# Performance work log

Measured on AMD Instinct MI355X. Metric: run time of the kernel, lower is better.

Reference implementation:

```python
import jax, jax.numpy as jnp
import numpy as np

K_BASE = 8
K_MAX = 20
NUM_GROUPS = 16  # min(32, 64 // 4)
EPS = 1e-5


def _knn_idx_adaptive(x, mask, k_base=K_BASE, k_max=K_MAX):
    # x: [B, N, D] float, mask: [B, N] bool. Returns idx: [B, N, k_max] int32.
    B, N, D = x.shape
    x2 = jnp.sum(x * x, axis=-1, keepdims=True)              # [B, N, 1]
    dist2 = x2 + x2.transpose(0, 2, 1) - 2.0 * jnp.einsum('bnd,bmd->bnm', x, x)
    dist2 = jnp.clip(dist2, 0.0)
    valid = mask[:, :, None] & mask[:, None, :]
    eye = jnp.eye(N, dtype=bool)[None]
    dist2 = jnp.where(valid & ~eye, dist2, jnp.inf)
    counts = mask.sum(axis=1)                                 # [B]
    k_per = jnp.clip(jnp.sqrt(counts.astype(jnp.float32) / 50.0) * k_base,
                     k_base, k_max).astype(jnp.int32)         # truncation == torch .long()
    k_global = jnp.minimum(k_max, jnp.maximum(1, counts.min() - 1))
    _, idx = jax.lax.top_k(-dist2, k_max)                     # [B, N, k_max]
    first_valid = jnp.argmax(mask, axis=1)                    # [B]
    cols = jnp.arange(k_max)[None, None, :]
    k_eff = jnp.minimum(k_per, k_global)[:, None, None]
    # cols < k_eff: true top-k neighbors; [k_eff, k_global): repeat first valid; >= k_global: pad 0
    idx = jnp.where(cols < k_eff, idx,
                    jnp.where(cols < k_global, first_valid[:, None, None], 0))
    return idx


def _group_norm(h, gamma, beta, num_groups=NUM_GROUPS, eps=EPS):
    # h: [..., C]
    shp = h.shape
    C = shp[-1]
    hg = h.reshape(shp[:-1] + (num_groups, C // num_groups))
    mu = hg.mean(axis=-1, keepdims=True)
    var = hg.var(axis=-1, keepdims=True)
    hg = (hg - mu) * jax.lax.rsqrt(var + eps)
    return hg.reshape(shp) * gamma + beta


def setup_inputs() -> dict:
    key = jax.random.key(0)
    kx, kl, k1, k2 = jax.random.split(key, 4)
    B, N, D, C = 16, 1024, 64, 64
    x = jax.random.normal(kx, (B, N, D), dtype=jnp.float32)
    lengths = jax.random.randint(kl, (B,), 256, N + 1)
    mask = jnp.arange(N)[None, :] < lengths[:, None]          # [B, N] bool
    W1 = jax.random.normal(k1, (2 * D, C), dtype=jnp.float32) / np.sqrt(2 * D)
    b1 = jnp.zeros((C,), dtype=jnp.float32)
    gamma = jnp.ones((C,), dtype=jnp.float32)
    beta = jnp.zeros((C,), dtype=jnp.float32)
    W2 = jax.random.normal(k2, (C, C), dtype=jnp.float32) / np.sqrt(C)
    b2 = jnp.zeros((C,), dtype=jnp.float32)
    return {"x": x, "mask": mask, "W1": W1, "b1": b1,
            "gamma": gamma, "beta": beta, "W2": W2, "b2": b2}


def reference(x, mask, W1, b1, gamma, beta, W2, b2):
    B, N, D = x.shape
    idx = _knn_idx_adaptive(x, mask)                          # [B, N, k]
    k = idx.shape[-1]
    x_nb = jnp.take_along_axis(x[:, :, None, :].repeat(1, axis=2),
                               idx[..., None], axis=1) if False else \
        x[jnp.arange(B)[:, None, None], idx]                  # [B, N, k, D]
    x_i = jnp.broadcast_to(x[:, :, None, :], (B, N, k, D))
    edge = jnp.concatenate([x_i, x_nb - x_i], axis=-1)        # [B, N, k, 2D]
    h = jax.nn.relu(_group_norm(edge @ W1 + b1, gamma, beta)) # [B, N, k, C]
    h = h @ W2 + b2
    out = h.max(axis=2)                                       # [B, N, C]
    return out * mask[..., None].astype(out.dtype)
```

## Files before the change

### kernel.cpp

```cpp
#include <hip/hip_runtime.h>
#include <stdint.h>

#define BB 16
#define NN 1024
#define DD 64
#define CC 64
#define KMAX 20
#define ROWS 8

typedef unsigned long long u64;
typedef float f32x2 __attribute__((ext_vector_type(2)));
typedef float f32x4v __attribute__((ext_vector_type(4)));
typedef short bf16x8 __attribute__((ext_vector_type(8)));

__device__ inline u64 umin64(u64 a, u64 b) { return a < b ? a : b; }

__device__ inline unsigned f2bf(float f) {
    unsigned u = __float_as_uint(f);
    return (u + 0x7FFFu + ((u >> 16) & 1u)) >> 16;
}

__device__ inline bf16x8 pack8(const float4 a, const float4 b) {
    union { unsigned u[4]; bf16x8 v; } r;
    r.u[0] = f2bf(a.x) | (f2bf(a.y) << 16);
    r.u[1] = f2bf(a.z) | (f2bf(a.w) << 16);
    r.u[2] = f2bf(b.x) | (f2bf(b.y) << 16);
    r.u[3] = f2bf(b.z) | (f2bf(b.w) << 16);
    return r.v;
}

struct bfpair { bf16x8 hi, lo; };
__device__ __forceinline__ bfpair split8(const float v[8]) {
    union { unsigned u[4]; bf16x8 x; } H, L;
#pragma unroll
    for (int i = 0; i < 4; ++i) {
        unsigned h0 = f2bf(v[2 * i]), h1 = f2bf(v[2 * i + 1]);
        float r0 = v[2 * i] - __uint_as_float(h0 << 16);
        float r1 = v[2 * i + 1] - __uint_as_float(h1 << 16);
        H.u[i] = h0 | (h1 << 16);
        L.u[i] = f2bf(r0) | (f2bf(r1) << 16);
    }
    bfpair r; r.hi = H.x; r.lo = L.x; return r;
}

__device__ inline void gn4(float4& h, const float4 g, const float4 be) {
    float mu = (h.x + h.y + h.z + h.w) * 0.25f;
    float dx = h.x - mu, dy = h.y - mu, dz = h.z - mu, dw = h.w - mu;
    float var = (dx * dx + dy * dy + dz * dz + dw * dw) * 0.25f;
    float rs = __builtin_amdgcn_rsqf(var + 1e-5f);
    h.x = fmaxf(fmaf(dx * rs, g.x, be.x), 0.f);
    h.y = fmaxf(fmaf(dy * rs, g.y, be.y), 0.f);
    h.z = fmaxf(fmaf(dz * rs, g.z, be.z), 0.f);
    h.w = fmaxf(fmaf(dw * rs, g.w, be.w), 0.f);
}

__global__ __launch_bounds__(256) void k1_all(const float* __restrict__ x,
                                              const float* __restrict__ W1,
                                              const float* __restrict__ b1,
                                              float* __restrict__ base,
                                              float* __restrict__ fb,
                                              float* __restrict__ xT,
                                              float* __restrict__ x2,
                                              const void* __restrict__ maskp,
                                              int* __restrict__ counts,
                                              int* __restrict__ keff) {
    __shared__ float sXT[16][65];
    __shared__ int scnt[BB];
    int w = threadIdx.x >> 6, lane = threadIdx.x & 63;
    int lg = lane >> 4, lr = lane & 15;
    int p0 = blockIdx.x * 16;

    float av[8];
    bfpair A[2];
    {
        const float* xr = x + (size_t)(p0 + lr) * DD;
#pragma unroll
        for (int kt = 0; kt < 2; ++kt) {
            float4 a0 = *(const float4*)(xr + kt * 32 + lg * 8);
            float4 a1 = *(const float4*)(xr + kt * 32 + lg * 8 + 4);
            av[0] = a0.x; av[1] = a0.y; av[2] = a0.z; av[3] = a0.w;
            av[4] = a1.x; av[5] = a1.y; av[6] = a1.z; av[7] = a1.w;
            A[kt] = split8(av);
        }
    }
    bfpair Wa[2], Wb[2];
#pragma unroll
    for (int kt = 0; kt < 2; ++kt) {
        const float* wpa = W1 + (size_t)(kt * 32 + lg * 8) * CC + w * 16 + lr;
        float wv[8];
#pragma unroll
        for (int e = 0; e < 8; ++e) wv[e] = wpa[e * CC];
        Wa[kt] = split8(wv);
        const float* wpb = wpa + (size_t)DD * CC;
#pragma unroll
        for (int e = 0; e < 8; ++e) wv[e] = wpb[e * CC];
        Wb[kt] = split8(wv);
    }
    f32x4v P = {0, 0, 0, 0}, Q = {0, 0, 0, 0};
#pragma unroll
    for (int kt = 0; kt < 2; ++kt) {
        P = __builtin_amdgcn_mfma_f32_16x16x32_bf16(A[kt].hi, Wa[kt].hi, P, 0, 0, 0);
        P = __builtin_amdgcn_mfma_f32_16x16x32_bf16(A[kt].hi, Wa[kt].lo, P, 0, 0, 0);
        P = __builtin_amdgcn_mfma_f32_16x16x32_bf16(A[kt].lo, Wa[kt].hi, P, 0, 0, 0);
        Q = __builtin_amdgcn_mfma_f32_16x16x32_bf16(A[kt].hi, Wb[kt].hi, Q, 0, 0, 0);
        Q = __builtin_amdgcn_mfma_f32_16x16x32_bf16(A[kt].hi, Wb[kt].lo, Q, 0, 0, 0);
        Q = __builtin_amdgcn_mfma_f32_16x16x32_bf16(A[kt].lo, Wb[kt].hi, Q, 0, 0, 0);
    }
    {
        float b1c = b1[w * 16 + lr];
#pragma unroll
        for (int r = 0; r < 4; ++r) {
            size_t off = (size_t)(p0 + lg * 4 + r) * CC + w * 16 + lr;
            base[off] = P[r] - Q[r] + b1c;
            fb[off] = Q[r];
        }
    }

#pragma unroll
    for (int q = 0; q < 4; ++q) {
        int pl = w * 4 + q;
        float xv = x[((size_t)(p0 + pl) << 6) + lane];
        sXT[pl][lane] = xv;
        float sq = xv * xv;
        for (int off = 32; off; off >>= 1) sq += __shfl_xor(sq, off);
        if (lane == 0) x2[p0 + pl] = sq;
    }
    __syncthreads();
    {
        int t = threadIdx.x;
        int b = p0 >> 10, nb = p0 & 1023;
        int d = t >> 2, q4 = (t & 3) << 2;
        float4 v;
        v.x = sXT[q4 + 0][d]; v.y = sXT[q4 + 1][d]; v.z = sXT[q4 + 2][d]; v.w = sXT[q4 + 3][d];
        *(float4*)&xT[(((size_t)(b << 6) + d) << 10) + nb + q4] = v;
    }

    if (blockIdx.x == 0) {
        const unsigned char* mb = (const unsigned char*)maskp;
        const int* mi = (const int*)maskp;
        bool bytelayout = (mb[1] != 0);
        for (int bq = 0; bq < 4; ++bq) {
            int bb = w * 4 + bq;
            int s = 0;
            for (int i = 0; i < 16; ++i) {
                int nn2 = lane + (i << 6);
                int v = bytelayout ? (mb[bb * NN + nn2] ? 1 : 0)
                                   : (mi[bb * NN + nn2] ? 1 : 0);
                s += v;
            }
            for (int off = 32; off; off >>= 1) s += __shfl_xor(s, off);
            if (lane == 0) scnt[bb] = s;
        }
        __syncthreads();
        int t = threadIdx.x;
        if (t < BB) {
            int minc = scnt[0];
            for (int qq = 1; qq < BB; ++qq) minc = min(minc, scnt[qq]);
            int kglob = min(KMAX, max(1, minc - 1));
            float c = (float)scnt[t];
            float v = sqrtf(c / 50.0f) * 8.0f;
            v = fminf(fmaxf(v, 8.0f), 20.0f);
            int kper = (int)v;
            counts[t] = scnt[t];
            keff[t] = min(kper, kglob);
        }
    }
}

#define CE(a, b)                                                      \
    {                                                                 \
        bool sw_ = pk[b] < pk[a];                                     \
        u64 ta_ = pk[a];                                              \
        pk[a] = sw_ ? pk[b] : pk[a];                                  \
        pk[b] = sw_ ? ta_ : pk[b];                                    \
    }

__device__ __forceinline__ u64 head16(const u64 (&pk)[16]) {
    u64 h01 = umin64(pk[0], pk[1]),   h23 = umin64(pk[2], pk[3]);
    u64 h45 = umin64(pk[4], pk[5]),   h67 = umin64(pk[6], pk[7]);
    u64 h89 = umin64(pk[8], pk[9]),   hab = umin64(pk[10], pk[11]);
    u64 hcd = umin64(pk[12], pk[13]), hef = umin64(pk[14], pk[15]);
    return umin64(umin64(umin64(h01, h23), umin64(h45, h67)),
                  umin64(umin64(h89, hab), umin64(hcd, hef)));
}

__device__ __forceinline__ int sortpop(u64 (&pk)[16], int kef, int lane) {
    CE(0,1) CE(2,3) CE(4,5) CE(6,7) CE(8,9) CE(10,11) CE(12,13) CE(14,15)
    CE(0,2) CE(1,3) CE(4,6) CE(5,7) CE(8,10) CE(9,11) CE(12,14) CE(13,15)
    CE(1,2) CE(5,6) CE(9,10) CE(13,14)
    CE(0,4) CE(1,5) CE(2,6) CE(3,7) CE(8,12) CE(9,13) CE(10,14) CE(11,15)
    CE(2,4) CE(3,5) CE(10,12) CE(11,13)
    CE(1,2) CE(3,4) CE(5,6) CE(9,10) CE(11,12) CE(13,14)
    CE(0,8) CE(1,9) CE(2,10) CE(3,11) CE(4,12) CE(5,13) CE(6,14) CE(7,15)
    CE(4,8) CE(5,9) CE(6,10) CE(7,11)
    CE(2,4) CE(3,5) CE(6,8) CE(7,9) CE(10,12) CE(11,13)
    CE(1,2) CE(3,4) CE(5,6) CE(7,8) CE(9,10) CE(11,12) CE(13,14)
    u64 myhead = pk[0];
    int my_m = 0;
    for (int j = 0; j < kef; ++j) {
        u64 g = myhead;
        for (int off = 32; off; off >>= 1) {
            u64 o = __shfl_xor(g, off);
            g = (o < g) ? o : g;
        }
        my_m = (j == lane) ? (int)(unsigned)(g & 0xffffffffu) : my_m;
        bool win = (myhead == g);
#pragma unroll
        for (int tt = 0; tt < 15; ++tt) pk[tt] = win ? pk[tt + 1] : pk[tt];
        pk[15] = win ? ~0ULL : pk[15];
        myhead = pk[0];
    }
    return my_m;
}

#define ROWFMA(r, rv, cv)                                                        \
    {                                                                            \
        axy[r] = __builtin_elementwise_fma((f32x2){rv, rv}, (f32x2){cv.x, cv.y}, \
                                           axy[r]);                              \
        azw[r] = __builtin_elementwise_fma((f32x2){rv, rv}, (f32x2){cv.z, cv.w}, \
                                           azw[r]);                              \
    }

__global__ __launch_bounds__(256) void k2_knn(const float* __restrict__ x,
                                              const float* __restrict__ xT,
                                              const float* __restrict__ x2,
                                              const int* __restrict__ counts,
                                              const int* __restrict__ keff,
                                              int* __restrict__ idx) {
    __shared__ float sD[ROWS][NN];
    int b = blockIdx.x >> 7;
    int n0 = (blockIdx.x & 127) * ROWS;
    int cnt = counts[b];
    if (n0 >= cnt) return;
    int kef = keff[b];
    int w = threadIdx.x >> 6, lane = threadIdx.x & 63;
    const float* x2b = x2 + (b << 10);

    if ((w << 8) < cnt) {
        f32x2 axy[ROWS], azw[ROWS];
#pragma unroll
        for (int r = 0; r < ROWS; ++r) { axy[r] = (f32x2){0.f, 0.f}; azw[r] = (f32x2){0.f, 0.f}; }
        const float* xTb = xT + ((size_t)b << 16);
        const float* xrow0 = x + ((size_t)(b << 10) + n0) * DD;
        int c0 = (w << 8) + (lane << 2);
        for (int d0 = 0; d0 < DD; d0 += 4) {
            float4 cv0 = *(const float4*)(xTb + ((size_t)(d0 + 0) << 10) + c0);
            float4 cv1 = *(const float4*)(xTb + ((size_t)(d0 + 1) << 10) + c0);
            float4 cv2 = *(const float4*)(xTb + ((size_t)(d0 + 2) << 10) + c0);
            float4 cv3 = *(const float4*)(xTb + ((size_t)(d0 + 3) << 10) + c0);
#pragma unroll
            for (int r = 0; r < ROWS; ++r) {
                float4 rv = *(const float4*)(xrow0 + r * DD + d0);
                ROWFMA(r, rv.x, cv0)
                ROWFMA(r, rv.y, cv1)
                ROWFMA(r, rv.z, cv2)
                ROWFMA(r, rv.w, cv3)
            }
        }
#pragma unroll
        for (int r = 0; r < ROWS; ++r)
            *(float4*)&sD[r][c0] = make_float4(axy[r].x, axy[r].y, azw[r].x, azw[r].y);
    }
    __syncthreads();

    int rA = w, rB = w + 4;
    int nA = n0 + rA, nB = n0 + rB;
    bool vA = nA < cnt, vB = nB < cnt;
    if (!vA) return;
    float x2A = x2b[nA];
    float x2B = x2b[nB & 1023];
    u64 pkA[16], pkB[16];
#pragma unroll
    for (int tt = 0; tt < 16; ++tt) {
        int c = (tt << 6) + lane;
        float xc = x2b[c];
        float dA = fmaxf((x2A + xc) - 2.0f * sD[rA][c], 0.0f);
        float dB = fmaxf((x2B + xc) - 2.0f * sD[rB][c], 0.0f);
        pkA[tt] = (c < cnt && c != nA)
            ? (((u64)__float_as_uint(dA) << 32) | (unsigned)c) : ~0ULL;
        pkB[tt] = (vB && c < cnt && c != nB)
            ? (((u64)__float_as_uint(dB) << 32) | (unsigned)c) : ~0ULL;
    }
    u64 hA = head16(pkA), hB = head16(pkB);
    unsigned hTA = (unsigned)(hA >> 48), hTB = (unsigned)(hB >> 48);
    unsigned prefA = 0u, prefB = 0u;
    int rankA = kef, rankB = kef;
#pragma unroll
    for (int bbit = 15; bbit >= 0; --bbit) {
        unsigned bitm = 1u << bbit;
        bool cA = (((hTA ^ prefA) >> (bbit + 1)) == 0) && ((hTA & bitm) == 0);
        bool cB = (((hTB ^ prefB) >> (bbit + 1)) == 0) && ((hTB & bitm) == 0);
        u64 mA = __ballot(cA);
        u64 mB = __ballot(cB);
        int nA0 = __popcll(mA), nB0 = __popcll(mB);
        if (rankA > nA0) { rankA -= nA0; prefA |= bitm; }
        if (rankB > nB0) { rankB -= nB0; prefB |= bitm; }
    }
    u64 t0A = ((u64)((prefA << 16) | 0xFFFFu) << 32) | 0xFFFFFFFFULL;
    u64 t0B = vB ? (((u64)((prefB << 16) | 0xFFFFu) << 32) | 0xFFFFFFFFULL) : 0ULL;

    u64* svA = (u64*)&sD[rA][0];
    u64* svB = (u64*)&sD[rB][0];
    u64 lmask = (lane == 0) ? 0ULL : ((~0ULL) >> (64 - lane));
    int SA = 0, SB = 0;
#pragma unroll
    for (int i = 0; i < 16; ++i) {
        bool qA = (pkA[i] <= t0A);
        bool qB = (pkB[i] <= t0B);
        u64 mA = __ballot(qA);
        u64 mB = __ballot(qB);
        if (qA) svA[SA + __popcll(mA & lmask)] = pkA[i];
        if (qB) svB[SB + __popcll(mB & lmask)] = pkB[i];
        SA += __popcll(mA);
        SB += __popcll(mB);
    }
    size_t prowA = (size_t)(b << 10) + nA;
    size_t prowB = (size_t)(b << 10) + nB;
    if (SA <= 64 && SB <= 64) {
        u64 sA = (lane < SA) ? svA[lane] : ~0ULL;
        u64 sB = (lane < SB) ? svB[lane] : ~0ULL;
        int rkA = 0, rkB = 0;
        int SM = max(SA, SB);
        for (int j = 0; j < SM; ++j) {
            u64 aj = svA[j];
            u64 bj = svB[j];
            rkA += (j < SA && aj < sA) ? 1 : 0;
            rkB += (j < SB && bj < sB) ? 1 : 0;
        }
        if (rkA < kef && lane < SA) idx[prowA * KMAX + rkA] = (int)(unsigned)(sA & 0xffffffffu);
        if (lane >= kef && lane < KMAX) idx[prowA * KMAX + lane] = 0;
        if (vB) {
            if (rkB < kef && lane < SB) idx[prowB * KMAX + rkB] = (int)(unsigned)(sB & 0xffffffffu);
            if (lane >= kef && lane < KMAX) idx[prowB * KMAX + lane] = 0;
        }
    } else {
        int mA = sortpop(pkA, kef, lane);
        if (lane < KMAX) idx[prowA * KMAX + lane] = (lane < kef) ? mA : 0;
        if (vB) {
            int mB = sortpop(pkB, kef, lane);
            if (lane < KMAX) idx[prowB * KMAX + lane] = (lane < kef) ? mB : 0;
        }
    }
}

__global__ __launch_bounds__(256, 2) void k3_mlp(const float* __restrict__ base,
                                                 const float* __restrict__ fb,
                                                 const int* __restrict__ idx,
                                                 const int* __restrict__ counts,
                                                 const float* __restrict__ gamma,
                                                 const float* __restrict__ beta,
                                                 const float* __restrict__ W2,
                                                 const float* __restrict__ b2,
                                                 float* __restrict__ out) {
    __shared__ float sC[4][64][20];
    int w = threadIdx.x >> 6, lane = threadIdx.x & 63;
    int lg = lane >> 4, lr = lane & 15;
    int p0 = blockIdx.x * 16;
    int b = p0 >> 10;
    int n0b = p0 & 1023;
    int cnt = counts[b];
    int pt = p0 + lr;
    bool aval = (n0b + lr) < cnt;

    bf16x8 Bf[4][2];
#pragma unroll
    for (int nt = 0; nt < 4; ++nt)
#pragma unroll
        for (int kt = 0; kt < 2; ++kt) {
            float4 lo, hi;
            const float* wp = W2 + (size_t)(kt * 32 + lg * 8) * CC + nt * 16 + lr;
            lo.x = wp[0 * CC]; lo.y = wp[1 * CC]; lo.z = wp[2 * CC]; lo.w = wp[3 * CC];
            hi.x = wp[4 * CC]; hi.y = wp[5 * CC]; hi.z = wp[6 * CC]; hi.w = wp[7 * CC];
            Bf[nt][kt] = pack8(lo, hi);
        }

    const float* bp = base + (size_t)pt * CC + lg * 8;
    float4 baA0 = *(const float4*)(bp);
    float4 baA1 = *(const float4*)(bp + 4);
    float4 baB0 = *(const float4*)(bp + 32);
    float4 baB1 = *(const float4*)(bp + 36);
    const float* gp = gamma + lg * 8;
    float4 gA0 = *(const float4*)(gp),      gA1 = *(const float4*)(gp + 4);
    float4 gB0 = *(const float4*)(gp + 32), gB1 = *(const float4*)(gp + 36);
    const float* bep = beta + lg * 8;
    float4 eA0 = *(const float4*)(bep),      eA1 = *(const float4*)(bep + 4);
    float4 eB0 = *(const float4*)(bep + 32), eB1 = *(const float4*)(bep + 36);

    const float* fbb = fb + ((size_t)(b << 10)) * CC;
    const int* idxp = idx + (size_t)pt * KMAX;

    f32x4v cmax[4];
#pragma unroll
    for (int nt = 0; nt < 4; ++nt) cmax[nt] = (f32x4v){-1e30f, -1e30f, -1e30f, -1e30f};

#pragma unroll
    for (int jj = 0; jj < 5; ++jj) {
        int j = w * 5 + jj;
        int m = aval ? idxp[j] : 0;
        const float* fr = fbb + (size_t)m * CC + lg * 8;
        float4 hA0 = *(const float4*)(fr);
        float4 hA1 = *(const float4*)(fr + 4);
        float4 hB0 = *(const float4*)(fr + 32);
        float4 hB1 = *(const float4*)(fr + 36);
        hA0.x += baA0.x; hA0.y += baA0.y; hA0.z += baA0.z; hA0.w += baA0.w;
        hA1.x += baA1.x; hA1.y += baA1.y; hA1.z += baA1.z; hA1.w += baA1.w;
        hB0.x += baB0.x; hB0.y += baB0.y; hB0.z += baB0.z; hB0.w += baB0.w;
        hB1.x += baB1.x; hB1.y += baB1.y; hB1.z += baB1.z; hB1.w += baB1.w;
        gn4(hA0, gA0, eA0);
        gn4(hA1, gA1, eA1);
        gn4(hB0, gB0, eB0);
        gn4(hB1, gB1, eB1);
        bf16x8 A0 = pack8(hA0, hA1);
        bf16x8 A1 = pack8(hB0, hB1);
#pragma unroll
        for (int nt = 0; nt < 4; ++nt) {
            f32x4v c = {0.f, 0.f, 0.f, 0.f};
            c = __builtin_amdgcn_mfma_f32_16x16x32_bf16(A0, Bf[nt][0], c, 0, 0, 0);
            c = __builtin_amdgcn_mfma_f32_16x16x32_bf16(A1, Bf[nt][1], c, 0, 0, 0);
            cmax[nt].x = fmaxf(cmax[nt].x, c.x);
            cmax[nt].y = fmaxf(cmax[nt].y, c.y);
            cmax[nt].z = fmaxf(cmax[nt].z, c.z);
            cmax[nt].w = fmaxf(cmax[nt].w, c.w);
        }
    }
#pragma unroll
    for (int nt = 0; nt < 4; ++nt)
        *(float4*)&sC[w][lane][nt * 4] = (float4){cmax[nt].x, cmax[nt].y, cmax[nt].z, cmax[nt].w};
    __syncthreads();
    float b2c = b2[lane];
#pragma unroll
    for (int q = 0; q < 4; ++q) {
        int R = w * 4 + q;
        int src = ((R >> 2) << 4) + lr;
        int reg = (lg << 2) + (R & 3);
        float v = fmaxf(fmaxf(sC[0][src][reg], sC[1][src][reg]),
                        fmaxf(sC[2][src][reg], sC[3][src][reg]));
        bool valid = (n0b + R) < cnt;
        out[(size_t)(p0 + R) * CC + lane] = valid ? (v + b2c) : 0.f;
    }
}

extern "C" void kernel_launch(void* const* d_in, const int* in_sizes, int n_in,
                              void* d_out, int out_size, void* d_ws, size_t ws_size,
                              hipStream_t stream) {
    const float* x     = (const float*)d_in[0];
    const void*  maskp = d_in[1];
    const float* W1    = (const float*)d_in[2];
    const float* b1    = (const float*)d_in[3];
    const float* gamma = (const float*)d_in[4];
    const float* beta  = (const float*)d_in[5];
    const float* W2    = (const float*)d_in[6];
    const float* b2    = (const float*)d_in[7];
    float* out = (float*)d_out;

    int* d_counts = (int*)d_ws;
    int* d_keff   = d_counts + 16;
    float* d_x2   = (float*)(d_counts + 32);
    float* d_base = d_x2 + BB * NN;
    float* d_fb   = d_base + (size_t)BB * NN * CC;
    int* d_idx    = (int*)(d_fb + (size_t)BB * NN * CC);
    float* d_xT   = (float*)d_out;

    hipLaunchKernelGGL(k1_all, dim3(BB * NN / 16), dim3(256), 0, stream,
                       x, W1, b1, d_base, d_fb, d_xT, d_x2, maskp, d_counts, d_keff);
    hipLaunchKernelGGL(k2_knn, dim3(BB * (NN / ROWS)), dim3(256), 0, stream,
                       x, d_xT, d_x2, d_counts, d_keff, d_idx);
    hipLaunchKernelGGL(k3_mlp, dim3(BB * NN / 16), dim3(256), 0, stream,
                       d_base, d_fb, d_idx, d_counts, gamma, beta, W2, b2, out);
}
```

Measured before the change: 88.38 us.

## Compute kNN distances with bf16-split MFMA and 16-bit keys, refine exactly

The kNN distance matrix is now computed with split-bf16 MFMA (hi/lo, three products) over 16-row tiles instead of scalar FMA on a transposed copy of x, so the transpose in the first kernel is dropped. Distances are stored in shared memory as truncated 16-bit keys. A radix threshold search on those keys picks candidates, and the candidates are re-ranked with exact fp32 dot products. This removes the xT traffic and puts the dot products on matrix cores, but adds a per-row refinement pass and a full exact fallback whenever more than 64 candidates survive.

New measurement: 118.6 us. +34.2%, slower.

```diff
diff --git a/kernel.cpp b/kernel.cpp
--- a/kernel.cpp
+++ b/kernel.cpp
@@ -6,14 +6,11 @@
 #define DD 64
 #define CC 64
 #define KMAX 20
-#define ROWS 8
 
 typedef unsigned long long u64;
 typedef float f32x2 __attribute__((ext_vector_type(2)));
 typedef float f32x4v __attribute__((ext_vector_type(4)));
 typedef short bf16x8 __attribute__((ext_vector_type(8)));
-
-__device__ inline u64 umin64(u64 a, u64 b) { return a < b ? a : b; }
 
 __device__ inline unsigned f2bf(float f) {
     unsigned u = __float_as_uint(f);
@@ -54,17 +51,15 @@
     h.w = fmaxf(fmaf(dw * rs, g.w, be.w), 0.f);
 }
 
-__global__ __launch_bounds__(256) void k1_all(const float* __restrict__ x,
-                                              const float* __restrict__ W1,
-                                              const float* __restrict__ b1,
-                                              float* __restrict__ base,
-                                              float* __restrict__ fb,
-                                              float* __restrict__ xT,
-                                              float* __restrict__ x2,
-                                              const void* __restrict__ maskp,
-                                              int* __restrict__ counts,
-                                              int* __restrict__ keff) {
-    __shared__ float sXT[16][65];
+__global__ __launch_bounds__(256) void k1a_feats(const float* __restrict__ x,
+                                                 const float* __restrict__ W1,
+                                                 const float* __restrict__ b1,
+                                                 float* __restrict__ base,
+                                                 float* __restrict__ fb,
+                                                 float* __restrict__ x2,
+                                                 const void* __restrict__ maskp,
+                                                 int* __restrict__ counts,
+                                                 int* __restrict__ keff) {
     __shared__ int scnt[BB];
     int w = threadIdx.x >> 6, lane = threadIdx.x & 63;
     int lg = lane >> 4, lr = lane & 15;
@@ -96,6 +91,7 @@
         for (int e = 0; e < 8; ++e) wv[e] = wpb[e * CC];
         Wb[kt] = split8(wv);
     }
+
     f32x4v P = {0, 0, 0, 0}, Q = {0, 0, 0, 0};
 #pragma unroll
     for (int kt = 0; kt < 2; ++kt) {
@@ -118,21 +114,11 @@
 
 #pragma unroll
     for (int q = 0; q < 4; ++q) {
-        int pl = w * 4 + q;
+        int pl = (w << 2) + q;
         float xv = x[((size_t)(p0 + pl) << 6) + lane];
-        sXT[pl][lane] = xv;
         float sq = xv * xv;
         for (int off = 32; off; off >>= 1) sq += __shfl_xor(sq, off);
         if (lane == 0) x2[p0 + pl] = sq;
-    }
-    __syncthreads();
-    {
-        int t = threadIdx.x;
-        int b = p0 >> 10, nb = p0 & 1023;
-        int d = t >> 2, q4 = (t & 3) << 2;
-        float4 v;
-        v.x = sXT[q4 + 0][d]; v.y = sXT[q4 + 1][d]; v.z = sXT[q4 + 2][d]; v.w = sXT[q4 + 3][d];
-        *(float4*)&xT[(((size_t)(b << 6) + d) << 10) + nb + q4] = v;
     }
 
     if (blockIdx.x == 0) {
@@ -174,15 +160,6 @@
         pk[a] = sw_ ? pk[b] : pk[a];                                  \
         pk[b] = sw_ ? ta_ : pk[b];                                    \
     }
-
-__device__ __forceinline__ u64 head16(const u64 (&pk)[16]) {
-    u64 h01 = umin64(pk[0], pk[1]),   h23 = umin64(pk[2], pk[3]);
-    u64 h45 = umin64(pk[4], pk[5]),   h67 = umin64(pk[6], pk[7]);
-    u64 h89 = umin64(pk[8], pk[9]),   hab = umin64(pk[10], pk[11]);
-    u64 hcd = umin64(pk[12], pk[13]), hef = umin64(pk[14], pk[15]);
-    return umin64(umin64(umin64(h01, h23), umin64(h45, h67)),
-                  umin64(umin64(h89, hab), umin64(hcd, hef)));
-}
 
 __device__ __forceinline__ int sortpop(u64 (&pk)[16], int kef, int lane) {
     CE(0,1) CE(2,3) CE(4,5) CE(6,7) CE(8,9) CE(10,11) CE(12,13) CE(14,15)
@@ -213,132 +190,178 @@
     return my_m;
 }
 
-#define ROWFMA(r, rv, cv)                                                        \
-    {                                                                            \
-        axy[r] = __builtin_elementwise_fma((f32x2){rv, rv}, (f32x2){cv.x, cv.y}, \
-                                           axy[r]);                              \
-        azw[r] = __builtin_elementwise_fma((f32x2){rv, rv}, (f32x2){cv.z, cv.w}, \
-                                           azw[r]);                              \
-    }
+__device__ __forceinline__ float exact_dist(const float* __restrict__ xrow_lds,
+                                            const float* __restrict__ xc,
+                                            float x2n, float x2c) {
+    float dot = 0.f;
+#pragma unroll
+    for (int d4 = 0; d4 < 16; ++d4) {
+        float4 cv = *(const float4*)(xc + (d4 << 2));
+        float4 rv = *(const float4*)(xrow_lds + (d4 << 2));
+        dot = fmaf(rv.x, cv.x, dot);
+        dot = fmaf(rv.y, cv.y, dot);
+        dot = fmaf(rv.z, cv.z, dot);
+        dot = fmaf(rv.w, cv.w, dot);
+    }
+    return fmaxf((x2n + x2c) - 2.0f * dot, 0.0f);
+}
 
 __global__ __launch_bounds__(256) void k2_knn(const float* __restrict__ x,
-                                              const float* __restrict__ xT,
                                               const float* __restrict__ x2,
                                               const int* __restrict__ counts,
                                               const int* __restrict__ keff,
                                               int* __restrict__ idx) {
-    __shared__ float sD[ROWS][NN];
-    int b = blockIdx.x >> 7;
-    int n0 = (blockIdx.x & 127) * ROWS;
+    __shared__ unsigned short sDa[NN][16];
+    __shared__ float sXrow[16][64];
+    __shared__ unsigned sSv[16][64];
+    __shared__ u64 sEx[16][64];
+    int b = blockIdx.x >> 6;
+    int n0 = (blockIdx.x & 63) << 4;
     int cnt = counts[b];
     if (n0 >= cnt) return;
     int kef = keff[b];
     int w = threadIdx.x >> 6, lane = threadIdx.x & 63;
+    int lg = lane >> 4, lr = lane & 15;
+    const float* xb = x + (((size_t)(b << 10)) << 6);
     const float* x2b = x2 + (b << 10);
 
+    {
+        int t = threadIdx.x;
+        int row = t >> 4, d4 = (t & 15) << 2;
+        *(float4*)&sXrow[row][d4] = *(const float4*)(xb + (size_t)(n0 + row) * DD + d4);
+    }
+
+    bfpair A[2];
+    {
+        const float* xr = xb + (size_t)(n0 + lr) * DD;
+        float av[8];
+#pragma unroll
+        for (int kt = 0; kt < 2; ++kt) {
+            float4 a0 = *(const float4*)(xr + kt * 32 + lg * 8);
+            float4 a1 = *(const float4*)(xr + kt * 32 + lg * 8 + 4);
+            av[0] = a0.x; av[1] = a0.y; av[2] = a0.z; av[3] = a0.w;
+            av[4] = a1.x; av[5] = a1.y; av[6] = a1.z; av[7] = a1.w;
+            A[kt] = split8(av);
+        }
+    }
+    float x2r[4];
+#pragma unroll
+    for (int r = 0; r < 4; ++r) x2r[r] = x2b[n0 + lg * 4 + r];
+
     if ((w << 8) < cnt) {
-        f32x2 axy[ROWS], azw[ROWS];
-#pragma unroll
-        for (int r = 0; r < ROWS; ++r) { axy[r] = (f32x2){0.f, 0.f}; azw[r] = (f32x2){0.f, 0.f}; }
-        const float* xTb = xT + ((size_t)b << 16);
-        const float* xrow0 = x + ((size_t)(b << 10) + n0) * DD;
-        int c0 = (w << 8) + (lane << 2);
-        for (int d0 = 0; d0 < DD; d0 += 4) {
-            float4 cv0 = *(const float4*)(xTb + ((size_t)(d0 + 0) << 10) + c0);
-            float4 cv1 = *(const float4*)(xTb + ((size_t)(d0 + 1) << 10) + c0);
-            float4 cv2 = *(const float4*)(xTb + ((size_t)(d0 + 2) << 10) + c0);
-            float4 cv3 = *(const float4*)(xTb + ((size_t)(d0 + 3) << 10) + c0);
-#pragma unroll
-            for (int r = 0; r < ROWS; ++r) {
-                float4 rv = *(const float4*)(xrow0 + r * DD + d0);
-                ROWFMA(r, rv.x, cv0)
-                ROWFMA(r, rv.y, cv1)
-                ROWFMA(r, rv.z, cv2)
-                ROWFMA(r, rv.w, cv3)
+        for (int tile = 0; tile < 16; ++tile) {
+            int c = (w << 8) + (tile << 4) + lr;
+            const float* xc = xb + (size_t)c * DD;
+            bfpair Bf[2];
+            float bv[8];
+#pragma unroll
+            for (int kt = 0; kt < 2; ++kt) {
+                float4 b0 = *(const float4*)(xc + kt * 32 + lg * 8);
+                float4 b1v = *(const float4*)(xc + kt * 32 + lg * 8 + 4);
+                bv[0] = b0.x; bv[1] = b0.y; bv[2] = b0.z; bv[3] = b0.w;
+                bv[4] = b1v.x; bv[5] = b1v.y; bv[6] = b1v.z; bv[7] = b1v.w;
+                Bf[kt] = split8(bv);
             }
-        }
-#pragma unroll
-        for (int r = 0; r < ROWS; ++r)
-            *(float4*)&sD[r][c0] = make_float4(axy[r].x, axy[r].y, azw[r].x, azw[r].y);
+            f32x4v D = {0, 0, 0, 0};
+#pragma unroll
+            for (int kt = 0; kt < 2; ++kt) {
+                D = __builtin_amdgcn_mfma_f32_16x16x32_bf16(A[kt].hi, Bf[kt].hi, D, 0, 0, 0);
+                D = __builtin_amdgcn_mfma_f32_16x16x32_bf16(A[kt].hi, Bf[kt].lo, D, 0, 0, 0);
+                D = __builtin_amdgcn_mfma_f32_16x16x32_bf16(A[kt].lo, Bf[kt].hi, D, 0, 0, 0);
+            }
+            float x2c = x2b[c];
+            u64 pk4 = 0;
+#pragma unroll
+            for (int r = 0; r < 4; ++r) {
+                float da = fmaxf((x2r[r] + x2c) - 2.0f * D[r], 0.0f);
+                pk4 |= (u64)(__float_as_uint(da) >> 16) << (16 * r);
+            }
+            *(u64*)&sDa[c][lg << 2] = pk4;
+        }
     }
     __syncthreads();
 
-    int rA = w, rB = w + 4;
-    int nA = n0 + rA, nB = n0 + rB;
-    bool vA = nA < cnt, vB = nB < cnt;
-    if (!vA) return;
-    float x2A = x2b[nA];
-    float x2B = x2b[nB & 1023];
-    u64 pkA[16], pkB[16];
+    u64 vv[16];
 #pragma unroll
     for (int tt = 0; tt < 16; ++tt) {
         int c = (tt << 6) + lane;
-        float xc = x2b[c];
-        float dA = fmaxf((x2A + xc) - 2.0f * sD[rA][c], 0.0f);
-        float dB = fmaxf((x2B + xc) - 2.0f * sD[rB][c], 0.0f);
-        pkA[tt] = (c < cnt && c != nA)
-            ? (((u64)__float_as_uint(dA) << 32) | (unsigned)c) : ~0ULL;
-        pkB[tt] = (vB && c < cnt && c != nB)
-            ? (((u64)__float_as_uint(dB) << 32) | (unsigned)c) : ~0ULL;
-    }
-    u64 hA = head16(pkA), hB = head16(pkB);
-    unsigned hTA = (unsigned)(hA >> 48), hTB = (unsigned)(hB >> 48);
-    unsigned prefA = 0u, prefB = 0u;
-    int rankA = kef, rankB = kef;
+        vv[tt] = *(const u64*)&sDa[c][w << 2];
+    }
+    unsigned hmin[4] = {0xFFFFu, 0xFFFFu, 0xFFFFu, 0xFFFFu};
+#pragma unroll
+    for (int tt = 0; tt < 16; ++tt) {
+        int c = (tt << 6) + lane;
+        bool cv = c < cnt;
+#pragma unroll
+        for (int r = 0; r < 4; ++r) {
+            int n_r = n0 + (w << 2) + r;
+            unsigned key = (unsigned)((vv[tt] >> (16 * r)) & 0xFFFFu);
+            bool ok = cv && (c != n_r);
+            hmin[r] = (ok && key < hmin[r]) ? key : hmin[r];
+        }
+    }
+    unsigned pref[4] = {0, 0, 0, 0};
+    int rnk[4] = {kef, kef, kef, kef};
 #pragma unroll
     for (int bbit = 15; bbit >= 0; --bbit) {
         unsigned bitm = 1u << bbit;
-        bool cA = (((hTA ^ prefA) >> (bbit + 1)) == 0) && ((hTA & bitm) == 0);
-        bool cB = (((hTB ^ prefB) >> (bbit + 1)) == 0) && ((hTB & bitm) == 0);
-        u64 mA = __ballot(cA);
-        u64 mB = __ballot(cB);
-        int nA0 = __popcll(mA), nB0 = __popcll(mB);
-        if (rankA > nA0) { rankA -= nA0; prefA |= bitm; }
-        if (rankB > nB0) { rankB -= nB0; prefB |= bitm; }
-    }
-    u64 t0A = ((u64)((prefA << 16) | 0xFFFFu) << 32) | 0xFFFFFFFFULL;
-    u64 t0B = vB ? (((u64)((prefB << 16) | 0xFFFFu) << 32) | 0xFFFFFFFFULL) : 0ULL;
-
-    u64* svA = (u64*)&sD[rA][0];
-    u64* svB = (u64*)&sD[rB][0];
+#pragma unroll
+        for (int r = 0; r < 4; ++r) {
+            bool cnd = (((hmin[r] ^ pref[r]) >> (bbit + 1)) == 0) && !(hmin[r] & bitm);
+            u64 m = __ballot(cnd);
+            int c0n = __popcll(m);
+            if (rnk[r] > c0n) { rnk[r] -= c0n; pref[r] |= bitm; }
+        }
+    }
+    unsigned thr16[4];
+#pragma unroll
+    for (int r = 0; r < 4; ++r) {
+        float tup = __uint_as_float((pref[r] << 16) | 0xFFFFu) + 1.0f;
+        thr16[r] = __float_as_uint(tup) >> 16;
+    }
     u64 lmask = (lane == 0) ? 0ULL : ((~0ULL) >> (64 - lane));
-    int SA = 0, SB = 0;
-#pragma unroll
-    for (int i = 0; i < 16; ++i) {
-        bool qA = (pkA[i] <= t0A);
-        bool qB = (pkB[i] <= t0B);
-        u64 mA = __ballot(qA);
-        u64 mB = __ballot(qB);
-        if (qA) svA[SA + __popcll(mA & lmask)] = pkA[i];
-        if (qB) svB[SB + __popcll(mB & lmask)] = pkB[i];
-        SA += __popcll(mA);
-        SB += __popcll(mB);
-    }
-    size_t prowA = (size_t)(b << 10) + nA;
-    size_t prowB = (size_t)(b << 10) + nB;
-    if (SA <= 64 && SB <= 64) {
-        u64 sA = (lane < SA) ? svA[lane] : ~0ULL;
-        u64 sB = (lane < SB) ? svB[lane] : ~0ULL;
-        int rkA = 0, rkB = 0;
-        int SM = max(SA, SB);
-        for (int j = 0; j < SM; ++j) {
-            u64 aj = svA[j];
-            u64 bj = svB[j];
-            rkA += (j < SA && aj < sA) ? 1 : 0;
-            rkB += (j < SB && bj < sB) ? 1 : 0;
-        }
-        if (rkA < kef && lane < SA) idx[prowA * KMAX + rkA] = (int)(unsigned)(sA & 0xffffffffu);
-        if (lane >= kef && lane < KMAX) idx[prowA * KMAX + lane] = 0;
-        if (vB) {
-            if (rkB < kef && lane < SB) idx[prowB * KMAX + rkB] = (int)(unsigned)(sB & 0xffffffffu);
-            if (lane >= kef && lane < KMAX) idx[prowB * KMAX + lane] = 0;
-        }
-    } else {
-        int mA = sortpop(pkA, kef, lane);
-        if (lane < KMAX) idx[prowA * KMAX + lane] = (lane < kef) ? mA : 0;
-        if (vB) {
-            int mB = sortpop(pkB, kef, lane);
-            if (lane < KMAX) idx[prowB * KMAX + lane] = (lane < kef) ? mB : 0;
+    int S[4] = {0, 0, 0, 0};
+#pragma unroll
+    for (int tt = 0; tt < 16; ++tt) {
+        int c = (tt << 6) + lane;
+        bool cv = c < cnt;
+#pragma unroll
+        for (int r = 0; r < 4; ++r) {
+            int n_r = n0 + (w << 2) + r;
+            unsigned key = (unsigned)((vv[tt] >> (16 * r)) & 0xFFFFu);
+            bool q = cv && (c != n_r) && (n_r < cnt) && (key <= thr16[r]);
+            u64 m = __ballot(q);
+            if (q) sSv[(w << 2) + r][S[r] + __popcll(m & lmask)] = (unsigned)c;
+            S[r] += __popcll(m);
+        }
+    }
+    for (int r = 0; r < 4; ++r) {
+        int rloc = (w << 2) + r;
+        int n_r = n0 + rloc;
+        if (n_r >= cnt) continue;
+        size_t prow = (size_t)(b << 10) + n_r;
+        int Sr = S[r];
+        float x2n = x2b[n_r];
+        if (Sr <= 64) {
+            int c = (lane < Sr) ? (int)sSv[rloc][lane] : 0;
+            float de = exact_dist(&sXrow[rloc][0], xb + (size_t)c * DD, x2n, x2b[c]);
+            u64 key = (lane < Sr) ? (((u64)__float_as_uint(de) << 32) | (unsigned)c)
+                                  : ~0ULL;
+            sEx[rloc][lane] = key;
+            int rk = 0;
+            for (int j = 0; j < Sr; ++j) rk += (sEx[rloc][j] < key) ? 1 : 0;
+            if (rk < kef && lane < Sr) idx[prow * KMAX + rk] = c;
+            if (lane >= kef && lane < KMAX) idx[prow * KMAX + lane] = 0;
+        } else {
+            u64 pk[16];
+            for (int tt = 0; tt < 16; ++tt) {
+                int c = (tt << 6) + lane;
+                float de = exact_dist(&sXrow[rloc][0], xb + (size_t)c * DD, x2n, x2b[c]);
+                pk[tt] = (c < cnt && c != n_r)
+                    ? (((u64)__float_as_uint(de) << 32) | (unsigned)c) : ~0ULL;
+            }
+            int mm = sortpop(pk, kef, lane);
+            if (lane < KMAX) idx[prow * KMAX + lane] = (lane < kef) ? mm : 0;
         }
     }
 }
@@ -459,12 +482,11 @@
     float* d_base = d_x2 + BB * NN;
     float* d_fb   = d_base + (size_t)BB * NN * CC;
     int* d_idx    = (int*)(d_fb + (size_t)BB * NN * CC);
-    float* d_xT   = (float*)d_out;
-
-    hipLaunchKernelGGL(k1_all, dim3(BB * NN / 16), dim3(256), 0, stream,
-                       x, W1, b1, d_base, d_fb, d_xT, d_x2, maskp, d_counts, d_keff);
-    hipLaunchKernelGGL(k2_knn, dim3(BB * (NN / ROWS)), dim3(256), 0, stream,
-                       x, d_xT, d_x2, d_counts, d_keff, d_idx);
+
+    hipLaunchKernelGGL(k1a_feats, dim3(BB * NN / 16), dim3(256), 0, stream,
+                       x, W1, b1, d_base, d_fb, d_x2, maskp, d_counts, d_keff);
+    hipLaunchKernelGGL(k2_knn, dim3(BB * (NN / 16)), dim3(256), 0, stream,
+                       x, d_x2, d_counts, d_keff, d_idx);
     hipLaunchKernelGGL(k3_mlp, dim3(BB * NN / 16), dim3(256), 0, stream,
                        d_base, d_fb, d_idx, d_counts, gamma, beta, W2, b2, out);
 }
```
